# Performance work log

Measured on AMD Instinct MI355X. Metric: run time of the kernel, lower is better.

Reference implementation:

```python
import jax, jax.numpy as jnp
import numpy as np

EPS = 1e-7
NUM_ROUTING = 3


def squash(s, axis=-1):
    # v = ||s||^2/(1+||s||^2) * s/||s||, numerically safe
    sq = jnp.sum(jnp.square(s), axis=axis, keepdims=True)
    scale = sq / (1.0 + sq) / jnp.sqrt(sq + EPS)
    return scale * s


def setup_inputs() -> dict:
    key = jax.random.key(0)
    k1, k2 = jax.random.split(key)
    B, IN_CAPS, IN_DIM = 256, 1152, 8
    NUM_CAPS, DIM_VEC = 10, 16
    inputs = jax.random.normal(k1, (B, IN_CAPS, IN_DIM), dtype=jnp.float32)
    # glorot_uniform over [in_caps, num_caps, dim_vec, in_dim]
    limit = np.sqrt(6.0 / (IN_DIM + DIM_VEC))
    W = jax.random.uniform(k2, (IN_CAPS, NUM_CAPS, DIM_VEC, IN_DIM), dtype=jnp.float32,
                           minval=-limit, maxval=limit)
    bias = jnp.zeros((IN_CAPS, NUM_CAPS), dtype=jnp.float32)
    return {"inputs": inputs, "W": W, "bias": bias}


def reference(inputs, W, bias):
    # u_hat[b,i,c,d] = W[i,c,d,e] @ inputs[b,i,e]
    u_hat = jnp.einsum('icde,bie->bicd', W, inputs)  # [B, in_caps, num_caps, dim_vec]
    b = bias[None]  # [1, in_caps, num_caps], broadcasts to [B, ...]
    for _ in range(NUM_ROUTING - 1):
        c = jax.nn.softmax(b, axis=2)                       # over num_capsule
        s = jnp.einsum('bic,bicd->bcd', c * jnp.ones_like(u_hat[..., 0]), u_hat)
        v = squash(s, axis=-1)                              # [B, num_caps, dim_vec]
        agreement = jnp.einsum('bicd,bcd->bic', u_hat, v)
        b = agreement + b + bias[None]
    c_last = jax.nn.softmax(b, axis=2)
    s = jnp.einsum('bic,bicd->bcd', c_last * jnp.ones_like(u_hat[..., 0]), u_hat)
    outputs = squash(s, axis=-1)                            # [B, num_caps, dim_vec]
    return outputs
```

## Files before the change

### kernel.cpp

```cpp
#include <hip/hip_runtime.h>
#include <math.h>

#define BATCH 256
#define IC    1152
#define EDIM  8
#define NC    10
#define DV    16

#define ITB   16
#define NSLAB (IC / ITB)
#define CDB   (NC * DV * BATCH)

__device__ __forceinline__ float dot8w(float4 w0, float4 w1, float4 a, float4 b) {
    float u = w0.x * a.x;
    u = fmaf(w0.y, a.y, u);
    u = fmaf(w0.z, a.z, u);
    u = fmaf(w0.w, a.w, u);
    u = fmaf(w1.x, b.x, u);
    u = fmaf(w1.y, b.y, u);
    u = fmaf(w1.z, b.z, u);
    u = fmaf(w1.w, b.w, u);
    return u;
}

__global__ __launch_bounds__(256)
void caps_xT(const float* __restrict__ x, const float* __restrict__ bias,
             float* __restrict__ xT, float* __restrict__ cw1)
{
    __shared__ float tile[16][132];
    const int t  = threadIdx.x;
    const int i0 = blockIdx.x * 16;
    const int b0 = blockIdx.y * 16;
    {
        const int b = t >> 4, i = t & 15;
        const float4* src = (const float4*)&x[((size_t)(b0 + b) * IC + i0 + i) * EDIM];
        float4 v0 = src[0], v1 = src[1];
        ((float4*)&tile[b][i * 8])[0] = v0;
        ((float4*)&tile[b][i * 8])[1] = v1;
    }
    if (blockIdx.y == 0 && t < 16 * NC) {
        const int i = i0 + t / NC;
        const int c = t - (t / NC) * NC;
        float ssum = 0.f, ec = 0.f;
        #pragma unroll
        for (int cc = 0; cc < NC; ++cc) {
            float e = __expf(bias[i * NC + cc]);
            ssum += e;
            if (cc == c) ec = e;
        }
        cw1[i * NC + c] = ec / ssum;
    }
    __syncthreads();
    {
        const int i = t >> 4, b = t & 15;
        float4 v0 = ((const float4*)&tile[b][i * 8])[0];
        float4 v1 = ((const float4*)&tile[b][i * 8])[1];
        float4* dst = (float4*)&xT[((size_t)(i0 + i) * BATCH + b0 + b) * EDIM];
        dst[0] = v0;
        dst[1] = v1;
    }
}

template<int MODE>
__global__ __launch_bounds__(256)
void caps_cw(const float* __restrict__ xT,
             const float* __restrict__ W,
             const float* __restrict__ bias,
             const float* __restrict__ vT1,
             const float* __restrict__ vT2,
             float* __restrict__ cw_g)
{
    __shared__ float4 sW[NC * DV * EDIM / 4];

    const int i = blockIdx.x;
    const int b = threadIdx.x;

    {
        const float4* Wg = (const float4*)(W + (size_t)i * NC * DV * EDIM);
        #pragma unroll
        for (int f = b; f < NC * DV * EDIM / 4; f += 256)
            sW[f] = Wg[f];
    }

    const float4 xv0 = ((const float4*)xT)[((size_t)i * BATCH + b) * 2 + 0];
    const float4 xv1 = ((const float4*)xT)[((size_t)i * BATCH + b) * 2 + 1];

    __syncthreads();

    float t2[NC];
    float t3[NC];

    #pragma unroll
    for (int c = 0; c < NC; ++c) {
        float a2 = 0.f, a3 = 0.f;
        #pragma unroll
        for (int d = 0; d < DV; ++d) {
            float4 w0 = sW[(c * DV + d) * 2 + 0];
            float4 w1 = sW[(c * DV + d) * 2 + 1];
            float u = dot8w(w0, w1, xv0, xv1);
            a2 = fmaf(u, vT1[(c * DV + d) * BATCH + b], a2);
            if (MODE == 3)
                a3 = fmaf(u, vT2[(c * DV + d) * BATCH + b], a3);
        }
        t2[c] = a2;
        if (MODE == 3) t3[c] = a3;
    }

    float ex[NC];
    float ssum = 0.f;
    #pragma unroll
    for (int c = 0; c < NC; ++c) {
        float bv = bias[i * NC + c];
        float logit = (MODE == 2) ? (t2[c] + 2.0f * bv)
                                  : (t3[c] + t2[c] + 3.0f * bv);
        ex[c] = __expf(logit);
        ssum += ex[c];
    }
    float inv = 1.0f / ssum;
    #pragma unroll
    for (int c = 0; c < NC; ++c)
        cw_g[((size_t)i * NC + c) * BATCH + b] = ex[c] * inv;
}

template<int FIRST>
__global__ __launch_bounds__(256)
void caps_wsum(const float* __restrict__ xT,
               const float* __restrict__ W,
               const float* __restrict__ cw1,
               const float* __restrict__ cw_g,
               float* __restrict__ slab)
{
    __shared__ float4 sW[ITB * 16];

    const int icb = blockIdx.x;
    const int c   = blockIdx.y;
    const int dh  = blockIdx.z;
    const int b   = threadIdx.x;
    const int i0  = icb * ITB;

    {
        const int row = b >> 4, col = b & 15;
        sW[b] = ((const float4*)W)[((size_t)(i0 + row) * NC + c) * (DV * EDIM / 4)
                                   + dh * 16 + col];
    }

    float s[8];
    #pragma unroll
    for (int q = 0; q < 8; ++q) s[q] = 0.f;

    __syncthreads();

    #pragma unroll 4
    for (int ii = 0; ii < ITB; ++ii) {
        const int i = i0 + ii;
        const float4 xv0 = ((const float4*)xT)[((size_t)i * BATCH + b) * 2 + 0];
        const float4 xv1 = ((const float4*)xT)[((size_t)i * BATCH + b) * 2 + 1];

        const float cw = FIRST ? cw1[i * NC + c]
                               : cw_g[((size_t)i * NC + c) * BATCH + b];

        #pragma unroll
        for (int q = 0; q < 8; ++q) {
            float4 w0 = sW[ii * 16 + q * 2 + 0];
            float4 w1 = sW[ii * 16 + q * 2 + 1];
            float u = dot8w(w0, w1, xv0, xv1);
            s[q] = fmaf(cw, u, s[q]);
        }
    }

    #pragma unroll
    for (int q = 0; q < 8; ++q)
        slab[(size_t)icb * CDB + (c * DV + dh * 8 + q) * BATCH + b] = s[q];
}

template<int LAST>
__global__ __launch_bounds__(1024)
void caps_squash(const float* __restrict__ slab, float* __restrict__ outp)
{
    __shared__ float part[4][DV][17];
    const int c  = blockIdx.x;
    const int bg = blockIdx.y;
    const int bs = threadIdx.x & 15;
    const int d  = (threadIdx.x >> 4) & 15;
    const int sg = threadIdx.x >> 8;
    const int b  = bg * 16 + bs;

    float a0 = 0.f, a1 = 0.f, a2 = 0.f;
    const int s0 = sg * 18;
    #pragma unroll
    for (int j = 0; j < 18; j += 3) {
        a0 += slab[(size_t)(s0 + j + 0) * CDB + (c * DV + d) * BATCH + b];
        a1 += slab[(size_t)(s0 + j + 1) * CDB + (c * DV + d) * BATCH + b];
        a2 += slab[(size_t)(s0 + j + 2) * CDB + (c * DV + d) * BATCH + b];
    }
    part[sg][d][bs] = (a0 + a1) + a2;
    __syncthreads();
    if (sg == 0)
        part[0][d][bs] = (part[0][d][bs] + part[1][d][bs])
                       + (part[2][d][bs] + part[3][d][bs]);
    __syncthreads();
    if (sg == 0) {
        float s = part[0][d][bs];
        float sq = 0.f;
        #pragma unroll
        for (int k = 0; k < DV; ++k) {
            float v = part[0][k][bs];
            sq = fmaf(v, v, sq);
        }
        float scale = sq / ((1.0f + sq) * sqrtf(sq + 1e-7f));
        float val = scale * s;
        if (LAST)
            outp[((size_t)b * NC + c) * DV + d] = val;
        else
            outp[(c * DV + d) * BATCH + b] = val;
    }
}

extern "C" void kernel_launch(void* const* d_in, const int* in_sizes, int n_in,
                              void* d_out, int out_size, void* d_ws, size_t ws_size,
                              hipStream_t stream)
{
    const float* x    = (const float*)d_in[0];
    const float* W    = (const float*)d_in[1];
    const float* bias = (const float*)d_in[2];
    float* out = (float*)d_out;

    float* ws   = (float*)d_ws;
    float* slab = ws;
    float* cw_g = slab + (size_t)NSLAB * CDB;
    float* vT1  = cw_g + (size_t)IC * NC * BATCH;
    float* vT2  = vT1 + NC * DV * BATCH;
    float* xT   = vT2 + NC * DV * BATCH;
    float* cw1  = xT + (size_t)IC * BATCH * EDIM;

    dim3 gT(IC / 16, BATCH / 16);
    dim3 gB(NSLAB, NC, 2);
    dim3 gS(NC, 16);

    caps_xT<<<gT, 256, 0, stream>>>(x, bias, xT, cw1);
    caps_wsum<1><<<gB, 256, 0, stream>>>(xT, W, cw1, cw_g, slab);
    caps_squash<0><<<gS, 1024, 0, stream>>>(slab, vT1);
    caps_cw<2><<<IC, 256, 0, stream>>>(xT, W, bias, vT1, vT1, cw_g);
    caps_wsum<0><<<gB, 256, 0, stream>>>(xT, W, cw1, cw_g, slab);
    caps_squash<0><<<gS, 1024, 0, stream>>>(slab, vT2);
    caps_cw<3><<<IC, 256, 0, stream>>>(xT, W, bias, vT1, vT2, cw_g);
    caps_wsum<0><<<gB, 256, 0, stream>>>(xT, W, cw1, cw_g, slab);
    caps_squash<1><<<gS, 1024, 0, stream>>>(slab, out);
}
```

Baseline: 193.7 us.

## Compute weighted sums with bf16 MFMA over prepacked weights and fewer K-splits

Replaces the scalar FMA weighted-sum kernel with a bf16 MFMA kernel. A new prep kernel converts W to bf16 in an MFMA-friendly layout. Each block folds the coupling coefficient into x, stages it in LDS, and splits K into 32 slabs, so the squash reduction now sums 32 partials instead of 72. The caps_cw kernel also drops its LDS staging of W and reads it directly from global memory. Rounding to bf16 reduces precision, and the weight conversion runs on every call.

```diff
diff --git a/kernel.cpp b/kernel.cpp
--- a/kernel.cpp
+++ b/kernel.cpp
@@ -7,20 +7,41 @@
 #define NC    10
 #define DV    16
 
-#define ITB   16
-#define NSLAB (IC / ITB)
-#define CDB   (NC * DV * BATCH)
+#define KS    32
+#define ITK   36
+#define IPP   12
+#define SLABSTRIDE (NC * DV * BATCH)
+
+typedef __attribute__((ext_vector_type(8))) __bf16 bf16x8;
+typedef __attribute__((ext_vector_type(8))) short short8;
+typedef __attribute__((ext_vector_type(4))) float f32x4;
+
+__device__ __forceinline__ short f2bf(float f) {
+    unsigned u = __float_as_uint(f);
+    return (short)((u + 0x7FFF + ((u >> 16) & 1)) >> 16);
+}
 
 __device__ __forceinline__ float dot8w(float4 w0, float4 w1, float4 a, float4 b) {
     float u = w0.x * a.x;
-    u = fmaf(w0.y, a.y, u);
-    u = fmaf(w0.z, a.z, u);
-    u = fmaf(w0.w, a.w, u);
-    u = fmaf(w1.x, b.x, u);
-    u = fmaf(w1.y, b.y, u);
-    u = fmaf(w1.z, b.z, u);
-    u = fmaf(w1.w, b.w, u);
+    u = fmaf(w0.y, a.y, u); u = fmaf(w0.z, a.z, u); u = fmaf(w0.w, a.w, u);
+    u = fmaf(w1.x, b.x, u); u = fmaf(w1.y, b.y, u);
+    u = fmaf(w1.z, b.z, u); u = fmaf(w1.w, b.w, u);
     return u;
+}
+
+__global__ __launch_bounds__(256)
+void caps_prepw(const float* __restrict__ W, short* __restrict__ Wb2)
+{
+    const int c = blockIdx.x;
+    const int d = blockIdx.y;
+    for (int i = threadIdx.x; i < IC; i += 256) {
+        const float4 w0 = ((const float4*)W)[(((size_t)i * NC + c) * DV + d) * 2 + 0];
+        const float4 w1 = ((const float4*)W)[(((size_t)i * NC + c) * DV + d) * 2 + 1];
+        short8 s;
+        s[0] = f2bf(w0.x); s[1] = f2bf(w0.y); s[2] = f2bf(w0.z); s[3] = f2bf(w0.w);
+        s[4] = f2bf(w1.x); s[5] = f2bf(w1.y); s[6] = f2bf(w1.z); s[7] = f2bf(w1.w);
+        *(short8*)&Wb2[((((size_t)c * 288 + (i >> 2)) * 64) + (i & 3) * 16 + d) * 8] = s;
+    }
 }
 
 __global__ __launch_bounds__(256)
@@ -70,23 +91,16 @@
              const float* __restrict__ vT2,
              float* __restrict__ cw_g)
 {
-    __shared__ float4 sW[NC * DV * EDIM / 4];
-
     const int i = blockIdx.x;
     const int b = threadIdx.x;
 
-    {
-        const float4* Wg = (const float4*)(W + (size_t)i * NC * DV * EDIM);
-        #pragma unroll
-        for (int f = b; f < NC * DV * EDIM / 4; f += 256)
-            sW[f] = Wg[f];
-    }
+    int voff = 0;
+    asm volatile("" : "+v"(voff));
+    const float4* Wg = (const float4*)(W + (size_t)i * NC * DV * EDIM);
 
     const float4 xv0 = ((const float4*)xT)[((size_t)i * BATCH + b) * 2 + 0];
     const float4 xv1 = ((const float4*)xT)[((size_t)i * BATCH + b) * 2 + 1];
 
-    __syncthreads();
-
     float t2[NC];
     float t3[NC];
 
@@ -95,8 +109,8 @@
         float a2 = 0.f, a3 = 0.f;
         #pragma unroll
         for (int d = 0; d < DV; ++d) {
-            float4 w0 = sW[(c * DV + d) * 2 + 0];
-            float4 w1 = sW[(c * DV + d) * 2 + 1];
+            float4 w0 = Wg[(c * DV + d) * 2 + 0 + voff];
+            float4 w1 = Wg[(c * DV + d) * 2 + 1 + voff];
             float u = dot8w(w0, w1, xv0, xv1);
             a2 = fmaf(u, vT1[(c * DV + d) * BATCH + b], a2);
             if (MODE == 3)
@@ -124,58 +138,77 @@
 
 template<int FIRST>
 __global__ __launch_bounds__(256)
-void caps_wsum(const float* __restrict__ xT,
-               const float* __restrict__ W,
-               const float* __restrict__ cw1,
-               const float* __restrict__ cw_g,
-               float* __restrict__ slab)
-{
-    __shared__ float4 sW[ITB * 16];
-
-    const int icb = blockIdx.x;
-    const int c   = blockIdx.y;
-    const int dh  = blockIdx.z;
-    const int b   = threadIdx.x;
-    const int i0  = icb * ITB;
-
-    {
-        const int row = b >> 4, col = b & 15;
-        sW[b] = ((const float4*)W)[((size_t)(i0 + row) * NC + c) * (DV * EDIM / 4)
-                                   + dh * 16 + col];
-    }
-
-    float s[8];
-    #pragma unroll
-    for (int q = 0; q < 8; ++q) s[q] = 0.f;
-
-    __syncthreads();
-
-    #pragma unroll 4
-    for (int ii = 0; ii < ITB; ++ii) {
-        const int i = i0 + ii;
-        const float4 xv0 = ((const float4*)xT)[((size_t)i * BATCH + b) * 2 + 0];
-        const float4 xv1 = ((const float4*)xT)[((size_t)i * BATCH + b) * 2 + 1];
-
-        const float cw = FIRST ? cw1[i * NC + c]
-                               : cw_g[((size_t)i * NC + c) * BATCH + b];
-
-        #pragma unroll
-        for (int q = 0; q < 8; ++q) {
-            float4 w0 = sW[ii * 16 + q * 2 + 0];
-            float4 w1 = sW[ii * 16 + q * 2 + 1];
-            float u = dot8w(w0, w1, xv0, xv1);
-            s[q] = fmaf(cw, u, s[q]);
-        }
-    }
-
-    #pragma unroll
-    for (int q = 0; q < 8; ++q)
-        slab[(size_t)icb * CDB + (c * DV + dh * 8 + q) * BATCH + b] = s[q];
+void caps_wsum_mfma(const float* __restrict__ xT,
+                    const short* __restrict__ Wb2,
+                    const float* __restrict__ cw1,
+                    const float* __restrict__ cw_g,
+                    float* __restrict__ s_part)
+{
+    __shared__ short B_lds[BATCH][104];
+
+    const int ks   = blockIdx.x;
+    const int c    = blockIdx.y;
+    const int tid  = threadIdx.x;
+    const int lane = tid & 63;
+    const int w    = tid >> 6;
+    const int i0   = ks * ITK;
+
+    f32x4 acc[4];
+    #pragma unroll
+    for (int t = 0; t < 4; ++t) acc[t] = (f32x4){0.f, 0.f, 0.f, 0.f};
+
+    const short8* Ag = (const short8*)Wb2;
+
+    #pragma unroll 1
+    for (int piece = 0; piece < 3; ++piece) {
+        {
+            const int b = tid;
+            #pragma unroll
+            for (int il = 0; il < IPP; ++il) {
+                const int i = i0 + piece * IPP + il;
+                float cwv = FIRST ? cw1[i * NC + c]
+                                  : cw_g[((size_t)i * NC + c) * BATCH + b];
+                const float4 x0 = ((const float4*)xT)[((size_t)i * BATCH + b) * 2 + 0];
+                const float4 x1 = ((const float4*)xT)[((size_t)i * BATCH + b) * 2 + 1];
+                short8 s;
+                s[0] = f2bf(cwv * x0.x); s[1] = f2bf(cwv * x0.y);
+                s[2] = f2bf(cwv * x0.z); s[3] = f2bf(cwv * x0.w);
+                s[4] = f2bf(cwv * x1.x); s[5] = f2bf(cwv * x1.y);
+                s[6] = f2bf(cwv * x1.z); s[7] = f2bf(cwv * x1.w);
+                *(short8*)&B_lds[b][il * 8] = s;
+            }
+        }
+        __syncthreads();
+        #pragma unroll
+        for (int kl = 0; kl < 3; ++kl) {
+            const int kg = ks * 9 + piece * 3 + kl;
+            short8 a8 = Ag[((size_t)c * 288 + kg) * 64 + lane];
+            bf16x8 af = __builtin_bit_cast(bf16x8, a8);
+            #pragma unroll
+            for (int t = 0; t < 4; ++t) {
+                const int brow = (w * 4 + t) * 16 + (lane & 15);
+                short8 b8 = *(const short8*)&B_lds[brow][kl * 32 + (lane >> 4) * 8];
+                bf16x8 bf = __builtin_bit_cast(bf16x8, b8);
+                acc[t] = __builtin_amdgcn_mfma_f32_16x16x32_bf16(af, bf, acc[t], 0, 0, 0);
+            }
+        }
+        __syncthreads();
+    }
+
+    #pragma unroll
+    for (int t = 0; t < 4; ++t) {
+        const int b = (w * 4 + t) * 16 + (lane & 15);
+        #pragma unroll
+        for (int r = 0; r < 4; ++r) {
+            const int d = (lane >> 4) * 4 + r;
+            s_part[(((size_t)ks * NC + c) * DV + d) * BATCH + b] = acc[t][r];
+        }
+    }
 }
 
 template<int LAST>
 __global__ __launch_bounds__(1024)
-void caps_squash(const float* __restrict__ slab, float* __restrict__ outp)
+void caps_squash(const float* __restrict__ s_part, float* __restrict__ outp)
 {
     __shared__ float part[4][DV][17];
     const int c  = blockIdx.x;
@@ -185,15 +218,13 @@
     const int sg = threadIdx.x >> 8;
     const int b  = bg * 16 + bs;
 
-    float a0 = 0.f, a1 = 0.f, a2 = 0.f;
-    const int s0 = sg * 18;
-    #pragma unroll
-    for (int j = 0; j < 18; j += 3) {
-        a0 += slab[(size_t)(s0 + j + 0) * CDB + (c * DV + d) * BATCH + b];
-        a1 += slab[(size_t)(s0 + j + 1) * CDB + (c * DV + d) * BATCH + b];
-        a2 += slab[(size_t)(s0 + j + 2) * CDB + (c * DV + d) * BATCH + b];
-    }
-    part[sg][d][bs] = (a0 + a1) + a2;
+    float a0 = 0.f, a1 = 0.f;
+    #pragma unroll
+    for (int j = 0; j < 8; j += 2) {
+        a0 += s_part[(((size_t)(sg * 8 + j + 0) * NC + c) * DV + d) * BATCH + b];
+        a1 += s_part[(((size_t)(sg * 8 + j + 1) * NC + c) * DV + d) * BATCH + b];
+    }
+    part[sg][d][bs] = a0 + a1;
     __syncthreads();
     if (sg == 0)
         part[0][d][bs] = (part[0][d][bs] + part[1][d][bs])
@@ -225,25 +256,28 @@
     const float* bias = (const float*)d_in[2];
     float* out = (float*)d_out;
 
-    float* ws   = (float*)d_ws;
-    float* slab = ws;
-    float* cw_g = slab + (size_t)NSLAB * CDB;
-    float* vT1  = cw_g + (size_t)IC * NC * BATCH;
-    float* vT2  = vT1 + NC * DV * BATCH;
-    float* xT   = vT2 + NC * DV * BATCH;
-    float* cw1  = xT + (size_t)IC * BATCH * EDIM;
+    float* ws     = (float*)d_ws;
+    float* s_part = ws;
+    float* cw_g   = s_part + (size_t)KS * SLABSTRIDE;
+    float* vT1    = cw_g + (size_t)IC * NC * BATCH;
+    float* vT2    = vT1 + NC * DV * BATCH;
+    float* xT     = vT2 + NC * DV * BATCH;
+    float* cw1    = xT + (size_t)IC * BATCH * EDIM;
+    short* Wb2    = (short*)(cw1 + IC * NC);
 
     dim3 gT(IC / 16, BATCH / 16);
-    dim3 gB(NSLAB, NC, 2);
+    dim3 gP(NC, DV);
+    dim3 gM(KS, NC);
     dim3 gS(NC, 16);
 
+    caps_prepw<<<gP, 256, 0, stream>>>(W, Wb2);
     caps_xT<<<gT, 256, 0, stream>>>(x, bias, xT, cw1);
-    caps_wsum<1><<<gB, 256, 0, stream>>>(xT, W, cw1, cw_g, slab);
-    caps_squash<0><<<gS, 1024, 0, stream>>>(slab, vT1);
+    caps_wsum_mfma<1><<<gM, 256, 0, stream>>>(xT, Wb2, cw1, cw_g, s_part);
+    caps_squash<0><<<gS, 1024, 0, stream>>>(s_part, vT1);
     caps_cw<2><<<IC, 256, 0, stream>>>(xT, W, bias, vT1, vT1, cw_g);
-    caps_wsum<0><<<gB, 256, 0, stream>>>(xT, W, cw1, cw_g, slab);
-    caps_squash<0><<<gS, 1024, 0, stream>>>(slab, vT2);
+    caps_wsum_mfma<0><<<gM, 256, 0, stream>>>(xT, Wb2, cw1, cw_g, s_part);
+    caps_squash<0><<<gS, 1024, 0, stream>>>(s_part, vT2);
     caps_cw<3><<<IC, 256, 0, stream>>>(xT, W, bias, vT1, vT2, cw_g);
-    caps_wsum<0><<<gB, 256, 0, stream>>>(xT, W, cw1, cw_g, slab);
-    caps_squash<1><<<gS, 1024, 0, stream>>>(slab, out);
-}
+    caps_wsum_mfma<0><<<gM, 256, 0, stream>>>(xT, Wb2, cw1, cw_g, s_part);
+    caps_squash<1><<<gS, 1024, 0, stream>>>(s_part, out);
+}
```

Result: slower. 238.2 us (+23.0%).
